# Optimization experiments

Hardware: AMD Instinct MI355X
Metric: run time of the kernel (lower is better)

Reference implementation:

```python
import jax, jax.numpy as jnp
import numpy as np

MAX_DISP = 4          # init kwarg
WIN = 2 * MAX_DISP + 1  # 9 -> 81 displacement offsets
CHUNK = 16            # hardcoded channel chunk size in the torch module


def setup_inputs() -> dict:
    key = jax.random.key(0)
    k1, k2 = jax.random.split(key)
    B, C, H, W = 8, 128, 96, 160
    x1 = jax.random.normal(k1, (B, C, H, W), dtype=jnp.float32)
    x2 = jax.random.normal(k2, (B, C, H, W), dtype=jnp.float32)
    return {"x1": x1, "x2": x2}


def reference(x1, x2):
    B, C, H, W = x2.shape
    pad = MAX_DISP
    # replicate padding == torch F.pad mode='replicate' == jnp 'edge'
    x2p = jnp.pad(x2, ((0, 0), (0, 0), (pad, pad), (pad, pad)), mode="edge")
    # offsets in the same row-major (dy outer, dx inner) order as the torch loops
    dy, dx = jnp.meshgrid(jnp.arange(-pad, pad + 1), jnp.arange(-pad, pad + 1), indexing="ij")
    offsets = jnp.stack([dy.ravel(), dx.ravel()], axis=1)  # [81, 2]
    num_chunks = -(-C // CHUNK)  # ceil(C/16); with C%16==0 chunk-mean == total-sum/num_chunks

    def body(carry, off):
        # shifted window of x2: x2p[:, :, pad+dy : pad+dy+H, pad+dx : pad+dx+W]
        sl = jax.lax.dynamic_slice(x2p, (0, 0, pad + off[0], pad + off[1]), (B, C, H, W))
        return carry, jnp.sum(x1 * sl, axis=1)  # [B, H, W]

    _, corr = jax.lax.scan(body, None, offsets)  # [81, B, H, W]
    corr = jnp.transpose(corr, (1, 0, 2, 3))     # [B, 81, H, W]
    return corr / jnp.asarray(num_chunks, corr.dtype)
```

## Files before the change

### kernel.cpp

```cpp
#include <hip/hip_runtime.h>
#include <cstdint>

#define BB 8
#define CC 128
#define HH 96
#define WW 160
#define HWsz (HH * WW)
#define TH 8
#define TW 32
#define CSTEP 8
#define HROWS 10
#define SW 48
#define CIW (HROWS * SW)
#define X2W (CSTEP * CIW)
#define X1W (CSTEP * TH * TW)
#define NWAVES 3
#define NTHREADS (NWAVES * 64)
#define NCHUNKS (CC / CSTEP)
#define NTILES (BB * (HH / TH) * (WW / TW))
#define NBLOCKS (NTILES * 3)
#define X1B (2 * X2W)

__device__ __forceinline__ void g2l_dword(const float* g, float* l) {
  __builtin_amdgcn_global_load_lds((const __attribute__((address_space(1))) void*)g,
                                   (__attribute__((address_space(3))) void*)l,
                                   4, 0, 0);
}

extern "C" __global__ void __launch_bounds__(NTHREADS, 2)
corr81_kernel(const float* __restrict__ x1, const float* __restrict__ x2,
              float* __restrict__ out)
{
  __shared__ __align__(16) float lds[2 * X2W + 2 * X1W];

  const int tid  = threadIdx.x;
  const int wvu  = __builtin_amdgcn_readfirstlane(tid >> 6);
  const int lane = tid & 63;
  const int r    = lane >> 3;
  const int j    = lane & 7;

  const int bid0 = blockIdx.x;
  const int bid  = (bid0 & 7) * (NBLOCKS / 8) + (bid0 >> 3);
  const int tile = bid / 3;
  const int g    = bid - 3 * tile;
  const int wt   = tile % (WW / TW);
  const int ht   = (tile / (WW / TW)) % (HH / TH);
  const int b    = tile / ((WW / TW) * (HH / TH));
  const int h0   = ht * TH;
  const int w0   = wt * TW;
  const int hb   = h0 + 3 * g - 4;

  int grw[HROWS];
#pragma unroll
  for (int rr = 0; rr < HROWS; ++rr) {
    int v = hb + rr; v = v < 0 ? 0 : (v > HH - 1 ? HH - 1 : v);
    grw[rr] = v * WW;
  }
  int sc2[3], dc2[3], sx1[3], dx1[3];
#pragma unroll
  for (int c = 0; c < 3; ++c) {
    int ci = 3 * wvu + c; if (ci >= CSTEP) ci = 6;
    sc2[c] = ci * HWsz;
    dc2[c] = ci * CIW;
    sx1[c] = ci * HWsz;
    dx1[c] = ci * (TH * TW);
  }
  int hqw[4];
#pragma unroll
  for (int q = 0; q < 4; ++q) hqw[q] = (h0 + 2 * q) * WW + w0;

  int gw[4];
#pragma unroll
  for (int mm = 0; mm < 4; ++mm) {
    const int cl = lane ^ (mm << 2);
    int v = w0 + cl - 4;
    gw[mm] = v < 0 ? 0 : (v > WW - 1 ? WW - 1 : v);
  }
  const int voff1 = (lane >> 5) * WW + (lane & 31);

  const float* x2b = x2 + (size_t)b * CC * HWsz;
  const float* x1b = x1 + (size_t)b * CC * HWsz;

  float acc[9][4];
#pragma unroll
  for (int d = 0; d < 9; ++d)
#pragma unroll
    for (int p = 0; p < 4; ++p) acc[d][p] = 0.f;

  const int R  = r + wvu;
  const int m  = R & 3;
  const int B0 = R * SW + (((j + 0) ^ m) << 2);
  const int B1 = R * SW + (((j + 1) ^ m) << 2);
  const int B2 = R * SW + (((j + 2) ^ m) << 2);
  const int abase = r * TW + 4 * j;

#define STAGE(BUF, S2, S1)                                                   \
  {                                                                          \
    float* d2 = &lds[(BUF) * X2W];                                           \
    float* d1 = &lds[X1B + (BUF) * X1W];                                     \
    if (lane < SW) {                                                         \
      _Pragma("unroll")                                                      \
      for (int i = 0; i < 30; ++i) {                                         \
        const int c = i / 10, row = i % 10;                                  \
        g2l_dword((S2) + sc2[c] + grw[row] + gw[row & 3],                    \
                  d2 + dc2[c] + row * SW);                                   \
      }                                                                      \
    }                                                                        \
    _Pragma("unroll")                                                        \
    for (int i = 0; i < 12; ++i) {                                           \
      const int c = i / 4, q = i % 4;                                        \
      g2l_dword((S1) + sx1[c] + hqw[q] + voff1, d1 + dx1[c] + q * 64);       \
    }                                                                        \
  }

#define COMPUTE(BUF)                                                         \
  {                                                                          \
    const float* xb = &lds[(BUF) * X2W];                                     \
    const float* ab = &lds[X1B + (BUF) * X1W] + abase;                       \
    _Pragma("unroll")                                                        \
    for (int ci = 0; ci < CSTEP; ++ci) {                                     \
      const float4 a4 = *(const float4*)(ab + ci * (TH * TW));               \
      const float4 f0 = *(const float4*)(xb + B0 + ci * CIW);                \
      const float4 f1 = *(const float4*)(xb + B1 + ci * CIW);                \
      const float4 f2 = *(const float4*)(xb + B2 + ci * CIW);                \
      const float av[4] = {a4.x, a4.y, a4.z, a4.w};                          \
      const float w12[12] = {f0.x, f0.y, f0.z, f0.w, f1.x, f1.y, f1.z,       \
                             f1.w, f2.x, f2.y, f2.z, f2.w};                  \
      _Pragma("unroll")                                                      \
      for (int d = 0; d < 9; ++d)                                            \
        _Pragma("unroll")                                                    \
        for (int p = 0; p < 4; ++p)                                          \
          acc[d][p] = fmaf(av[p], w12[d + p], acc[d][p]);                    \
    }                                                                        \
  }

  STAGE(0, x2b, x1b)

#pragma unroll 1
  for (int k = 0; k < NCHUNKS - 1; ++k) {
    {
      const float* s2 = x2b + (size_t)(k + 1) * (CSTEP * HWsz);
      const float* s1 = x1b + (size_t)(k + 1) * (CSTEP * HWsz);
      STAGE((k + 1) & 1, s2, s1)
    }

    __builtin_amdgcn_sched_barrier(0);
    asm volatile("s_waitcnt vmcnt(42)" ::: "memory");
    __builtin_amdgcn_sched_barrier(0);
    __builtin_amdgcn_s_barrier();
    __builtin_amdgcn_sched_barrier(0);

    COMPUTE(k & 1)

    __builtin_amdgcn_sched_barrier(0);
    __builtin_amdgcn_s_barrier();
    __builtin_amdgcn_sched_barrier(0);
  }

  asm volatile("s_waitcnt vmcnt(0)" ::: "memory");
  __builtin_amdgcn_sched_barrier(0);
  __builtin_amdgcn_s_barrier();
  __builtin_amdgcn_sched_barrier(0);
  COMPUTE((NCHUNKS - 1) & 1)

  const int dy = 3 * g + wvu;
  float* op = out + (((size_t)b * 81 + (size_t)dy * 9) * HH + (h0 + r)) * WW + (w0 + 4 * j);
#pragma unroll
  for (int d = 0; d < 9; ++d) {
    float4 v;
    v.x = acc[d][0] * 0.125f;
    v.y = acc[d][1] * 0.125f;
    v.z = acc[d][2] * 0.125f;
    v.w = acc[d][3] * 0.125f;
    *(float4*)(op + (size_t)d * HWsz) = v;
  }
}

extern "C" void kernel_launch(void* const* d_in, const int* in_sizes, int n_in,
                              void* d_out, int out_size, void* d_ws, size_t ws_size,
                              hipStream_t stream) {
  const float* x1 = (const float*)d_in[0];
  const float* x2 = (const float*)d_in[1];
  float* out = (float*)d_out;
  corr81_kernel<<<dim3(NBLOCKS), dim3(NTHREADS), 0, stream>>>(x1, x2, out);
}
```

Baseline: 210.9 us.

## Give each lane 8 pixels over half the channels and reduce halves with a shuffle

Each lane now computes 8 output pixels for 9 dx offsets, but only over half of each channel chunk. The two wave halves split the channels and combine their partial sums with a cross-half shuffle before the store. The x1 staging layout gets an XOR swizzle to keep LDS float4 reads conflict-free. This raises FMAs per LDS read, which cuts LDS traffic per FLOP, at the cost of doubling accumulator registers (72 floats), which could pressure occupancy under launch bounds of 2.

```diff
diff --git a/kernel.cpp b/kernel.cpp
--- a/kernel.cpp
+++ b/kernel.cpp
@@ -36,8 +36,9 @@
   const int tid  = threadIdx.x;
   const int wvu  = __builtin_amdgcn_readfirstlane(tid >> 6);
   const int lane = tid & 63;
-  const int r    = lane >> 3;
-  const int j    = lane & 7;
+  const int h    = lane >> 5;
+  const int r    = (lane >> 2) & 7;
+  const int s    = lane & 3;
 
   const int bid0 = blockIdx.x;
   const int bid  = (bid0 & 7) * (NBLOCKS / 8) + (bid0 >> 3);
@@ -76,23 +77,30 @@
     int v = w0 + cl - 4;
     gw[mm] = v < 0 ? 0 : (v > WW - 1 ? WW - 1 : v);
   }
-  const int voff1 = (lane >> 5) * WW + (lane & 31);
+  {
+  }
+  const int hi1 = lane >> 5, lo1 = lane & 31;
+  const int voffE = hi1 * WW + (lo1 ^ (hi1 << 2));
+  const int voffO = hi1 * WW + (lo1 ^ ((2 | hi1) << 2));
 
   const float* x2b = x2 + (size_t)b * CC * HWsz;
   const float* x1b = x1 + (size_t)b * CC * HWsz;
 
-  float acc[9][4];
+  float acc[9][8];
 #pragma unroll
   for (int d = 0; d < 9; ++d)
 #pragma unroll
-    for (int p = 0; p < 4; ++p) acc[d][p] = 0.f;
+    for (int p = 0; p < 8; ++p) acc[d][p] = 0.f;
 
   const int R  = r + wvu;
-  const int m  = R & 3;
-  const int B0 = R * SW + (((j + 0) ^ m) << 2);
-  const int B1 = R * SW + (((j + 1) ^ m) << 2);
-  const int B2 = R * SW + (((j + 2) ^ m) << 2);
-  const int abase = r * TW + 4 * j;
+  const int m2 = R & 3;
+  int B4[4];
+#pragma unroll
+  for (int t = 0; t < 4; ++t)
+    B4[t] = h * (4 * CIW) + R * SW + (((2 * s + t) ^ m2) << 2);
+  const int m1 = r & 3;
+  const int A0 = h * 1024 + r * TW + (((2 * s + 0) ^ m1) << 2);
+  const int A1 = h * 1024 + r * TW + (((2 * s + 1) ^ m1) << 2);
 
 #define STAGE(BUF, S2, S1)                                                   \
   {                                                                          \
@@ -109,28 +117,32 @@
     _Pragma("unroll")                                                        \
     for (int i = 0; i < 12; ++i) {                                           \
       const int c = i / 4, q = i % 4;                                        \
-      g2l_dword((S1) + sx1[c] + hqw[q] + voff1, d1 + dx1[c] + q * 64);       \
+      g2l_dword((S1) + sx1[c] + hqw[q] + ((q & 1) ? voffO : voffE),          \
+                d1 + dx1[c] + q * 64);                                       \
     }                                                                        \
   }
 
 #define COMPUTE(BUF)                                                         \
   {                                                                          \
     const float* xb = &lds[(BUF) * X2W];                                     \
-    const float* ab = &lds[X1B + (BUF) * X1W] + abase;                       \
+    const float* ab = &lds[X1B + (BUF) * X1W];                               \
     _Pragma("unroll")                                                        \
-    for (int ci = 0; ci < CSTEP; ++ci) {                                     \
-      const float4 a4 = *(const float4*)(ab + ci * (TH * TW));               \
-      const float4 f0 = *(const float4*)(xb + B0 + ci * CIW);                \
-      const float4 f1 = *(const float4*)(xb + B1 + ci * CIW);                \
-      const float4 f2 = *(const float4*)(xb + B2 + ci * CIW);                \
-      const float av[4] = {a4.x, a4.y, a4.z, a4.w};                          \
-      const float w12[12] = {f0.x, f0.y, f0.z, f0.w, f1.x, f1.y, f1.z,       \
-                             f1.w, f2.x, f2.y, f2.z, f2.w};                  \
+    for (int q = 0; q < 4; ++q) {                           \
+      const float4 a0 = *(const float4*)(ab + A0 + q * 256);                 \
+      const float4 a1 = *(const float4*)(ab + A1 + q * 256);                 \
+      const float av[8] = {a0.x, a0.y, a0.z, a0.w, a1.x, a1.y, a1.z, a1.w};  \
+      float w16[16];                                                         \
+      _Pragma("unroll")                                                      \
+      for (int t = 0; t < 4; ++t) {                                          \
+        const float4 f = *(const float4*)(xb + B4[t] + q * CIW);             \
+        w16[4*t+0] = f.x; w16[4*t+1] = f.y;                                  \
+        w16[4*t+2] = f.z; w16[4*t+3] = f.w;                                  \
+      }                                                                      \
       _Pragma("unroll")                                                      \
       for (int d = 0; d < 9; ++d)                                            \
         _Pragma("unroll")                                                    \
-        for (int p = 0; p < 4; ++p)                                          \
-          acc[d][p] = fmaf(av[p], w12[d + p], acc[d][p]);                    \
+        for (int p = 0; p < 8; ++p)                                          \
+          acc[d][p] = fmaf(av[p], w16[d + p], acc[d][p]);                    \
     }                                                                        \
   }
 
@@ -164,14 +176,23 @@
   COMPUTE((NCHUNKS - 1) & 1)
 
   const int dy = 3 * g + wvu;
-  float* op = out + (((size_t)b * 81 + (size_t)dy * 9) * HH + (h0 + r)) * WW + (w0 + 4 * j);
+  float* op = out + (((size_t)b * 81 + (size_t)dy * 9) * HH + (h0 + r)) * WW
+                  + (w0 + 8 * s + 4 * h);
 #pragma unroll
   for (int d = 0; d < 9; ++d) {
+    const float own0 = h ? acc[d][4] : acc[d][0];
+    const float own1 = h ? acc[d][5] : acc[d][1];
+    const float own2 = h ? acc[d][6] : acc[d][2];
+    const float own3 = h ? acc[d][7] : acc[d][3];
+    const float snd0 = h ? acc[d][0] : acc[d][4];
+    const float snd1 = h ? acc[d][1] : acc[d][5];
+    const float snd2 = h ? acc[d][2] : acc[d][6];
+    const float snd3 = h ? acc[d][3] : acc[d][7];
     float4 v;
-    v.x = acc[d][0] * 0.125f;
-    v.y = acc[d][1] * 0.125f;
-    v.z = acc[d][2] * 0.125f;
-    v.w = acc[d][3] * 0.125f;
+    v.x = (own0 + __shfl_xor(snd0, 32)) * 0.125f;
+    v.y = (own1 + __shfl_xor(snd1, 32)) * 0.125f;
+    v.z = (own2 + __shfl_xor(snd2, 32)) * 0.125f;
+    v.w = (own3 + __shfl_xor(snd3, 32)) * 0.125f;
     *(float4*)(op + (size_t)d * HWsz) = v;
   }
 }
```

Measured after the change: 205.9 us. 1.02x faster.

## Give each wave private LDS buffers and load x1 straight into registers

Applied to the files above, without the earlier changes.

The x2 staging is reorganised so each wave keeps its own double-buffered LDS region holding only the 8 rows its dy offset needs. That removes every block-level s_barrier from the channel loop. The x1 tile is no longer staged through LDS: each lane prefetches its float4 values directly from global memory into registers for the next chunk. The trade is more global/L2 traffic, since the three waves now re-load overlapping x2 rows and identical x1 data, plus a larger LDS footprint per block.

```diff
diff --git a/kernel.cpp b/kernel.cpp
--- a/kernel.cpp
+++ b/kernel.cpp
@@ -9,17 +9,15 @@
 #define TH 8
 #define TW 32
 #define CSTEP 8
-#define HROWS 10
 #define SW 48
-#define CIW (HROWS * SW)
-#define X2W (CSTEP * CIW)
-#define X1W (CSTEP * TH * TW)
+#define CIW (TH * SW)
+#define BUFW (CSTEP * CIW)
+#define WAVEW (2 * BUFW)
 #define NWAVES 3
 #define NTHREADS (NWAVES * 64)
 #define NCHUNKS (CC / CSTEP)
 #define NTILES (BB * (HH / TH) * (WW / TW))
 #define NBLOCKS (NTILES * 3)
-#define X1B (2 * X2W)
 
 __device__ __forceinline__ void g2l_dword(const float* g, float* l) {
   __builtin_amdgcn_global_load_lds((const __attribute__((address_space(1))) void*)g,
@@ -31,7 +29,7 @@
 corr81_kernel(const float* __restrict__ x1, const float* __restrict__ x2,
               float* __restrict__ out)
 {
-  __shared__ __align__(16) float lds[2 * X2W + 2 * X1W];
+  __shared__ __align__(16) float lds[NWAVES * WAVEW];
 
   const int tid  = threadIdx.x;
   const int wvu  = __builtin_amdgcn_readfirstlane(tid >> 6);
@@ -48,27 +46,15 @@
   const int b    = tile / ((WW / TW) * (HH / TH));
   const int h0   = ht * TH;
   const int w0   = wt * TW;
-  const int hb   = h0 + 3 * g - 4;
+  const int dy   = 3 * g + wvu;
 
-  int grw[HROWS];
+  int grw[TH];
 #pragma unroll
-  for (int rr = 0; rr < HROWS; ++rr) {
-    int v = hb + rr; v = v < 0 ? 0 : (v > HH - 1 ? HH - 1 : v);
-    grw[rr] = v * WW;
+  for (int row = 0; row < TH; ++row) {
+    int v = h0 + dy - 4 + row;
+    v = v < 0 ? 0 : (v > HH - 1 ? HH - 1 : v);
+    grw[row] = v * WW;
   }
-  int sc2[3], dc2[3], sx1[3], dx1[3];
-#pragma unroll
-  for (int c = 0; c < 3; ++c) {
-    int ci = 3 * wvu + c; if (ci >= CSTEP) ci = 6;
-    sc2[c] = ci * HWsz;
-    dc2[c] = ci * CIW;
-    sx1[c] = ci * HWsz;
-    dx1[c] = ci * (TH * TW);
-  }
-  int hqw[4];
-#pragma unroll
-  for (int q = 0; q < 4; ++q) hqw[q] = (h0 + 2 * q) * WW + w0;
-
   int gw[4];
 #pragma unroll
   for (int mm = 0; mm < 4; ++mm) {
@@ -76,10 +62,11 @@
     int v = w0 + cl - 4;
     gw[mm] = v < 0 ? 0 : (v > WW - 1 ? WW - 1 : v);
   }
-  const int voff1 = (lane >> 5) * WW + (lane & 31);
 
+  float* wb = &lds[wvu * WAVEW];
   const float* x2b = x2 + (size_t)b * CC * HWsz;
-  const float* x1b = x1 + (size_t)b * CC * HWsz;
+  const float* x1c = x1 + (size_t)b * CC * HWsz
+                        + (size_t)(h0 + r) * WW + (w0 + 4 * j);
 
   float acc[9][4];
 #pragma unroll
@@ -87,43 +74,38 @@
 #pragma unroll
     for (int p = 0; p < 4; ++p) acc[d][p] = 0.f;
 
-  const int R  = r + wvu;
-  const int m  = R & 3;
-  const int B0 = R * SW + (((j + 0) ^ m) << 2);
-  const int B1 = R * SW + (((j + 1) ^ m) << 2);
-  const int B2 = R * SW + (((j + 2) ^ m) << 2);
-  const int abase = r * TW + 4 * j;
+  const int m  = r & 3;
+  const int B0 = r * SW + (((j + 0) ^ m) << 2);
+  const int B1 = r * SW + (((j + 1) ^ m) << 2);
+  const int B2 = r * SW + (((j + 2) ^ m) << 2);
 
-#define STAGE(BUF, S2, S1)                                                   \
-  {                                                                          \
-    float* d2 = &lds[(BUF) * X2W];                                           \
-    float* d1 = &lds[X1B + (BUF) * X1W];                                     \
-    if (lane < SW) {                                                         \
-      _Pragma("unroll")                                                      \
-      for (int i = 0; i < 30; ++i) {                                         \
-        const int c = i / 10, row = i % 10;                                  \
-        g2l_dword((S2) + sc2[c] + grw[row] + gw[row & 3],                    \
-                  d2 + dc2[c] + row * SW);                                   \
-      }                                                                      \
-    }                                                                        \
+#define STG(BUF, SRC, LO, HI)                                                \
+  if (lane < SW) {                                                          \
     _Pragma("unroll")                                                        \
-    for (int i = 0; i < 12; ++i) {                                           \
-      const int c = i / 4, q = i % 4;                                        \
-      g2l_dword((S1) + sx1[c] + hqw[q] + voff1, d1 + dx1[c] + q * 64);       \
+    for (int i = (LO); i < (HI); ++i) {                                      \
+      const int ci = i >> 3, row = i & 7;                                    \
+      g2l_dword((SRC) + ci * HWsz + grw[row] + gw[row & 3],                  \
+                wb + (BUF) * BUFW + ci * CIW + row * SW);                    \
     }                                                                        \
   }
 
-#define COMPUTE(BUF)                                                         \
+#define PFL(KP)                                                              \
   {                                                                          \
-    const float* xb = &lds[(BUF) * X2W];                                     \
-    const float* ab = &lds[X1B + (BUF) * X1W] + abase;                       \
+    const float* xp = x1c + (size_t)(KP) * (CSTEP * HWsz);                   \
+    _Pragma("unroll")                                                        \
+    for (int q = 0; q < CSTEP; ++q)                                          \
+      pf[q] = *(const float4*)(xp + (size_t)q * HWsz);                       \
+  }
+
+#define COMPUTE(CB)                                                          \
+  {                                                                          \
+    const float* xb = wb + (CB) * BUFW;                                      \
     _Pragma("unroll")                                                        \
     for (int ci = 0; ci < CSTEP; ++ci) {                                     \
-      const float4 a4 = *(const float4*)(ab + ci * (TH * TW));               \
-      const float4 f0 = *(const float4*)(xb + B0 + ci * CIW);                \
-      const float4 f1 = *(const float4*)(xb + B1 + ci * CIW);                \
-      const float4 f2 = *(const float4*)(xb + B2 + ci * CIW);                \
-      const float av[4] = {a4.x, a4.y, a4.z, a4.w};                          \
+      const float av[4] = {pf[ci].x, pf[ci].y, pf[ci].z, pf[ci].w};          \
+      const float4 f0 = *(const float4*)(xb + ci * CIW + B0);                \
+      const float4 f1 = *(const float4*)(xb + ci * CIW + B1);                \
+      const float4 f2 = *(const float4*)(xb + ci * CIW + B2);                \
       const float w12[12] = {f0.x, f0.y, f0.z, f0.w, f1.x, f1.y, f1.z,       \
                              f1.w, f2.x, f2.y, f2.z, f2.w};                  \
       _Pragma("unroll")                                                      \
@@ -134,36 +116,33 @@
     }                                                                        \
   }
 
-  STAGE(0, x2b, x1b)
+  float4 pf[CSTEP];
+
+  STG(0, x2b, 0, 64)
+  PFL(0)
 
 #pragma unroll 1
   for (int k = 0; k < NCHUNKS - 1; ++k) {
-    {
-      const float* s2 = x2b + (size_t)(k + 1) * (CSTEP * HWsz);
-      const float* s1 = x1b + (size_t)(k + 1) * (CSTEP * HWsz);
-      STAGE((k + 1) & 1, s2, s1)
-    }
+    const float* s2 = x2b + (size_t)(k + 1) * (CSTEP * HWsz);
+    const int nb = (k + 1) & 1;
 
     __builtin_amdgcn_sched_barrier(0);
-    asm volatile("s_waitcnt vmcnt(42)" ::: "memory");
+    STG(nb, s2, 0, 32)
     __builtin_amdgcn_sched_barrier(0);
-    __builtin_amdgcn_s_barrier();
+    asm volatile("s_waitcnt vmcnt(32)" ::: "memory");
+    __builtin_amdgcn_sched_barrier(0);
+    STG(nb, s2, 32, 64)
     __builtin_amdgcn_sched_barrier(0);
 
     COMPUTE(k & 1)
-
-    __builtin_amdgcn_sched_barrier(0);
-    __builtin_amdgcn_s_barrier();
+    PFL(k + 1)
     __builtin_amdgcn_sched_barrier(0);
   }
 
   asm volatile("s_waitcnt vmcnt(0)" ::: "memory");
   __builtin_amdgcn_sched_barrier(0);
-  __builtin_amdgcn_s_barrier();
-  __builtin_amdgcn_sched_barrier(0);
   COMPUTE((NCHUNKS - 1) & 1)
 
-  const int dy = 3 * g + wvu;
   float* op = out + (((size_t)b * 81 + (size_t)dy * 9) * HH + (h0 + r)) * WW + (w0 + 4 * j);
 #pragma unroll
   for (int d = 0; d < 9; ++d) {
```

Measured after the change: 233.7 us. +10.8%, slower.

## Load x1 directly into registers with one-chunk prefetch instead of LDS staging

Applied to the files above, without the earlier changes.

Stops staging x1 tiles through shared memory. Each thread now loads its own float4 of x1 per channel straight from global memory into registers, prefetching the next chunk after the current compute. This drops the LDS footprint and the x1 LDS reads, and the wait count and schedule barriers are adjusted to match. The trade-off is that each wave now fetches x1 separately (more L2 traffic) and needs extra VGPRs for the prefetch buffer.

```diff
diff --git a/kernel.cpp b/kernel.cpp
--- a/kernel.cpp
+++ b/kernel.cpp
@@ -13,13 +13,11 @@
 #define SW 48
 #define CIW (HROWS * SW)
 #define X2W (CSTEP * CIW)
-#define X1W (CSTEP * TH * TW)
 #define NWAVES 3
 #define NTHREADS (NWAVES * 64)
 #define NCHUNKS (CC / CSTEP)
 #define NTILES (BB * (HH / TH) * (WW / TW))
 #define NBLOCKS (NTILES * 3)
-#define X1B (2 * X2W)
 
 __device__ __forceinline__ void g2l_dword(const float* g, float* l) {
   __builtin_amdgcn_global_load_lds((const __attribute__((address_space(1))) void*)g,
@@ -31,7 +29,7 @@
 corr81_kernel(const float* __restrict__ x1, const float* __restrict__ x2,
               float* __restrict__ out)
 {
-  __shared__ __align__(16) float lds[2 * X2W + 2 * X1W];
+  __shared__ __align__(16) float lds[2 * X2W];
 
   const int tid  = threadIdx.x;
   const int wvu  = __builtin_amdgcn_readfirstlane(tid >> 6);
@@ -56,18 +54,13 @@
     int v = hb + rr; v = v < 0 ? 0 : (v > HH - 1 ? HH - 1 : v);
     grw[rr] = v * WW;
   }
-  int sc2[3], dc2[3], sx1[3], dx1[3];
+  int sc2[3], dc2[3];
 #pragma unroll
   for (int c = 0; c < 3; ++c) {
     int ci = 3 * wvu + c; if (ci >= CSTEP) ci = 6;
     sc2[c] = ci * HWsz;
     dc2[c] = ci * CIW;
-    sx1[c] = ci * HWsz;
-    dx1[c] = ci * (TH * TW);
   }
-  int hqw[4];
-#pragma unroll
-  for (int q = 0; q < 4; ++q) hqw[q] = (h0 + 2 * q) * WW + w0;
 
   int gw[4];
 #pragma unroll
@@ -76,10 +69,10 @@
     int v = w0 + cl - 4;
     gw[mm] = v < 0 ? 0 : (v > WW - 1 ? WW - 1 : v);
   }
-  const int voff1 = (lane >> 5) * WW + (lane & 31);
 
   const float* x2b = x2 + (size_t)b * CC * HWsz;
-  const float* x1b = x1 + (size_t)b * CC * HWsz;
+  const float* x1c = x1 + (size_t)b * CC * HWsz
+                        + (size_t)(h0 + r) * WW + (w0 + 4 * j);
 
   float acc[9][4];
 #pragma unroll
@@ -92,38 +85,35 @@
   const int B0 = R * SW + (((j + 0) ^ m) << 2);
   const int B1 = R * SW + (((j + 1) ^ m) << 2);
   const int B2 = R * SW + (((j + 2) ^ m) << 2);
-  const int abase = r * TW + 4 * j;
 
-#define STAGE(BUF, S2, S1)                                                   \
-  {                                                                          \
+#define STAGE(BUF, S2)                                                       \
+  if (lane < SW) {                                                          \
     float* d2 = &lds[(BUF) * X2W];                                           \
-    float* d1 = &lds[X1B + (BUF) * X1W];                                     \
-    if (lane < SW) {                                                         \
-      _Pragma("unroll")                                                      \
-      for (int i = 0; i < 30; ++i) {                                         \
-        const int c = i / 10, row = i % 10;                                  \
-        g2l_dword((S2) + sc2[c] + grw[row] + gw[row & 3],                    \
-                  d2 + dc2[c] + row * SW);                                   \
-      }                                                                      \
-    }                                                                        \
     _Pragma("unroll")                                                        \
-    for (int i = 0; i < 12; ++i) {                                           \
-      const int c = i / 4, q = i % 4;                                        \
-      g2l_dword((S1) + sx1[c] + hqw[q] + voff1, d1 + dx1[c] + q * 64);       \
+    for (int i = 0; i < 30; ++i) {                                           \
+      const int c = i / 10, row = i % 10;                                    \
+      g2l_dword((S2) + sc2[c] + grw[row] + gw[row & 3],                      \
+                d2 + dc2[c] + row * SW);                                     \
     }                                                                        \
   }
 
-#define COMPUTE(BUF)                                                         \
+#define PFL(KP)                                                              \
   {                                                                          \
-    const float* xb = &lds[(BUF) * X2W];                                     \
-    const float* ab = &lds[X1B + (BUF) * X1W] + abase;                       \
+    const float* xp = x1c + (size_t)(KP) * (CSTEP * HWsz);                   \
+    _Pragma("unroll")                                                        \
+    for (int q = 0; q < CSTEP; ++q)                                          \
+      pf[q] = *(const float4*)(xp + (size_t)q * HWsz);                       \
+  }
+
+#define COMPUTE(CB)                                                          \
+  {                                                                          \
+    const float* xb = &lds[(CB) * X2W];                                      \
     _Pragma("unroll")                                                        \
     for (int ci = 0; ci < CSTEP; ++ci) {                                     \
-      const float4 a4 = *(const float4*)(ab + ci * (TH * TW));               \
+      const float av[4] = {pf[ci].x, pf[ci].y, pf[ci].z, pf[ci].w};          \
       const float4 f0 = *(const float4*)(xb + B0 + ci * CIW);                \
       const float4 f1 = *(const float4*)(xb + B1 + ci * CIW);                \
       const float4 f2 = *(const float4*)(xb + B2 + ci * CIW);                \
-      const float av[4] = {a4.x, a4.y, a4.z, a4.w};                          \
       const float w12[12] = {f0.x, f0.y, f0.z, f0.w, f1.x, f1.y, f1.z,       \
                              f1.w, f2.x, f2.y, f2.z, f2.w};                  \
       _Pragma("unroll")                                                      \
@@ -134,25 +124,29 @@
     }                                                                        \
   }
 
-  STAGE(0, x2b, x1b)
+  float4 pf[CSTEP];
+
+  STAGE(0, x2b)
+  PFL(0)
 
 #pragma unroll 1
   for (int k = 0; k < NCHUNKS - 1; ++k) {
     {
       const float* s2 = x2b + (size_t)(k + 1) * (CSTEP * HWsz);
-      const float* s1 = x1b + (size_t)(k + 1) * (CSTEP * HWsz);
-      STAGE((k + 1) & 1, s2, s1)
+      __builtin_amdgcn_sched_barrier(0);
+      STAGE((k + 1) & 1, s2)
+      __builtin_amdgcn_sched_barrier(0);
     }
 
-    __builtin_amdgcn_sched_barrier(0);
-    asm volatile("s_waitcnt vmcnt(42)" ::: "memory");
+    asm volatile("s_waitcnt vmcnt(38)" ::: "memory");
     __builtin_amdgcn_sched_barrier(0);
     __builtin_amdgcn_s_barrier();
     __builtin_amdgcn_sched_barrier(0);
 
     COMPUTE(k & 1)
+    PFL(k + 1)
+    __builtin_amdgcn_sched_barrier(0);
 
-    __builtin_amdgcn_sched_barrier(0);
     __builtin_amdgcn_s_barrier();
     __builtin_amdgcn_sched_barrier(0);
   }
@@ -161,7 +155,7 @@
   __builtin_amdgcn_sched_barrier(0);
   __builtin_amdgcn_s_barrier();
   __builtin_amdgcn_sched_barrier(0);
-  COMPUTE((NCHUNKS - 1) & 1)
+  COMPUTE(1)
 
   const int dy = 3 * g + wvu;
   float* op = out + (((size_t)b * 81 + (size_t)dy * 9) * HH + (h0 + r)) * WW + (w0 + 4 * j);
```

Result: slower. 216.6 us (+2.7%).
